# Kernel tuning notes

Hardware: AMD Instinct MI355X
Metric: run time of the kernel (lower is better)

## Reference

```python
import jax, jax.numpy as jnp
import numpy as np

E = 16          # expert_num
T = 8192        # token_num
H = 1024        # hidden_size
I = 4096        # intermediate_size
LN_EPS = 1e-12


def setup_inputs() -> dict:
    key = jax.random.key(0)
    ks = jax.random.split(key, 6)
    hidden_states = jax.random.normal(ks[0], (T, H), dtype=jnp.float32)
    perm = jax.random.permutation(ks[1], T).astype(jnp.int32)
    s1 = 1.0 / np.sqrt(H)
    s2 = 1.0 / np.sqrt(I)
    w1 = jax.random.uniform(ks[2], (E, I, H), jnp.float32, -s1, s1)
    b1 = jax.random.uniform(ks[3], (E, I), jnp.float32, -s1, s1)
    w2 = jax.random.uniform(ks[4], (E, H, I), jnp.float32, -s2, s2)
    b2 = jax.random.uniform(ks[5], (E, H), jnp.float32, -s2, s2)
    ln_gamma = jnp.ones((H,), jnp.float32)
    ln_beta = jnp.zeros((H,), jnp.float32)
    return {"hidden_states": hidden_states, "perm": perm, "w1": w1, "b1": b1,
            "w2": w2, "b2": b2, "ln_gamma": ln_gamma, "ln_beta": ln_beta}


def _layer_norm(x, gamma, beta, eps):
    mu = jnp.mean(x, axis=-1, keepdims=True)
    var = jnp.var(x, axis=-1, keepdims=True)
    return (x - mu) * jax.lax.rsqrt(var + eps) * gamma + beta


def reference(hidden_states, perm, w1, b1, w2, b2, ln_gamma, ln_beta):
    # dispatch: gather tokens by random permutation, group per expert
    xp = hidden_states[perm].reshape(E, T // E, H)            # [E, T/E, H]
    # grouped expert FFN (batched GEMM replaces the per-expert Python loop)
    h = jnp.einsum('eth,eih->eti', xp, w1) + b1[:, None, :]   # [E, T/E, I]
    h = jax.nn.gelu(h, approximate=False)
    o = jnp.einsum('eti,ehi->eth', h, w2) + b2[:, None, :]    # [E, T/E, H]
    # scatter-restore via inverse permutation
    restore = jnp.argsort(perm)
    o = o.reshape(T, H)[restore]
    # dropout is identity (p=0, eval); residual + LayerNorm
    return _layer_norm(o + hidden_states, ln_gamma, ln_beta, LN_EPS)
```

## Files before the change

### kernel.cpp

```cpp
#include <hip/hip_runtime.h>
#include <hip/hip_bf16.h>
#include <stdint.h>

#define E_NUM 16
#define T_NUM 8192
#define H_DIM 1024
#define I_DIM 4096
#define MPE   512

typedef __attribute__((ext_vector_type(8))) short short8;
typedef __attribute__((ext_vector_type(4))) float f32x4;
using bf16 = __hip_bfloat16;

typedef const __attribute__((address_space(1))) void GLV;
typedef __attribute__((address_space(3))) void LDSV;

__device__ __forceinline__ uint32_t pack2_bf16(float a, float b) {
  union { float f; uint32_t u; } ua, ub;
  ua.f = a; ub.f = b;
  uint32_t x = ua.u + (0x7FFFu + ((ua.u >> 16) & 1u));
  uint32_t y = ub.u + (0x7FFFu + ((ub.u >> 16) & 1u));
  return (x >> 16) | (y & 0xFFFF0000u);
}

__device__ __forceinline__ short8 cvt8(f32x4 a, f32x4 b) {
  union { short8 s; __hip_bfloat162 h[4]; } r;
  r.h[0] = __float22bfloat162_rn({a[0], a[1]});
  r.h[1] = __float22bfloat162_rn({a[2], a[3]});
  r.h[2] = __float22bfloat162_rn({b[0], b[1]});
  r.h[3] = __float22bfloat162_rn({b[2], b[3]});
  return r.s;
}

__device__ __forceinline__ float fast_gelu(float x) {
  const float p = x * fmaf(x * x, -0.0713548162726f, -1.59576912161f);
  return x * __builtin_amdgcn_rcpf(1.0f + __expf(p));
}

__global__ __launch_bounds__(256)
void gather_cast_kernel(const float* __restrict__ hs, const int* __restrict__ perm,
                        uint32_t* __restrict__ xp) {
  const int r = blockIdx.x;
  const int t = threadIdx.x;
  const int src = perm[r];
  float4 v = ((const float4*)(hs + (size_t)src * H_DIM))[t];
  uint2 o;
  o.x = pack2_bf16(v.x, v.y);
  o.y = pack2_bf16(v.z, v.w);
  ((uint2*)(xp + (size_t)r * (H_DIM / 2)))[t] = o;
}

template<int LOG_NBN, int NWG>
__global__ __launch_bounds__(512, 2)
void moe_g1_kernel(const bf16* __restrict__ A, const float* __restrict__ Bw,
                   const float* __restrict__ bias, bf16* __restrict__ Hout) {
  constexpr int N = I_DIM, K = H_DIM;
  constexpr int NK = K / 32;
  __shared__ bf16  As[2][128 * 64];
  __shared__ float Bs[2][128 * 32];

  constexpr int qx = NWG >> 3;
  const int orig = blockIdx.x;
  const int wg = (orig & 7) * qx + (orig >> 3);
  const int bm = wg & 1;
  const int bn = (wg >> 1) & ((1 << LOG_NBN) - 1);
  const int e  = wg >> (1 + LOG_NBN);

  const int tid = threadIdx.x;
  const int l = tid & 63;
  const int wv = tid >> 6;
  const int wr = wv >> 1, wc = wv & 1;
  const int fr = l & 15, fq = l >> 4;
  const int rx = fr & 7;

  const bf16*  Ae = A  + ((size_t)e * MPE + (size_t)bm * 256) * K;
  const float* Be = Bw + ((size_t)e * N + (size_t)bn * 128) * K;

  const int p0 = tid >> 3;
  const int ga = (tid & 7) ^ (p0 & 7);
  const bf16* As0 = Ae + (size_t)(p0      + 128 * (ga >> 2)) * K + (ga & 3) * 8;
  const bf16* As1 = Ae + (size_t)(p0 + 64 + 128 * (ga >> 2)) * K + (ga & 3) * 8;
  const float* Bs0 = Be + (size_t)p0 * K + ga * 4;
  const float* Bs1 = Be + (size_t)(p0 + 64) * K + ga * 4;

#define STAGE1(buf, kt)                                                            \
  {                                                                                \
    __builtin_amdgcn_global_load_lds((GLV*)(As0 + (kt) * 32),                      \
        (LDSV*)((char*)&As[buf][0] + tid * 16), 16, 0, 0);                         \
    __builtin_amdgcn_global_load_lds((GLV*)(As1 + (kt) * 32),                      \
        (LDSV*)((char*)&As[buf][0] + 8192 + tid * 16), 16, 0, 0);                  \
    __builtin_amdgcn_global_load_lds((GLV*)(Bs0 + (kt) * 32),                      \
        (LDSV*)((char*)&Bs[buf][0] + tid * 16), 16, 0, 0);                         \
    __builtin_amdgcn_global_load_lds((GLV*)(Bs1 + (kt) * 32),                      \
        (LDSV*)((char*)&Bs[buf][0] + 8192 + tid * 16), 16, 0, 0);                  \
  }

  const int aoff  = ((wr & 1) * 64 + fr) * 128 + ((((wr >> 1) << 2) | fq) ^ rx) * 16;
  const int b0off = (wc * 64 + fr) * 128 + (((fq << 1)) ^ rx) * 16;
  const int b1off = (wc * 64 + fr) * 128 + (((fq << 1) | 1) ^ rx) * 16;

  f32x4 acc[4][4];
#pragma unroll
  for (int m = 0; m < 4; ++m)
#pragma unroll
    for (int n = 0; n < 4; ++n) acc[m][n] = (f32x4){0.f, 0.f, 0.f, 0.f};

  STAGE1(0, 0);
  __syncthreads();

  for (int t = 0; t < NK; ++t) {
    const int cur = t & 1;
    if (t + 1 < NK) STAGE1(cur ^ 1, t + 1);

    short8 a8[4];
#pragma unroll
    for (int m = 0; m < 4; ++m)
      a8[m] = *(const short8*)((const char*)&As[cur][0] + aoff + m * 2048);
    short8 b8[4];
#pragma unroll
    for (int n = 0; n < 4; ++n) {
      const f32x4 x0 = *(const f32x4*)((const char*)&Bs[cur][0] + b0off + n * 2048);
      const f32x4 x1 = *(const f32x4*)((const char*)&Bs[cur][0] + b1off + n * 2048);
      b8[n] = cvt8(x0, x1);
    }
#pragma unroll
    for (int m = 0; m < 4; ++m)
#pragma unroll
      for (int n = 0; n < 4; ++n)
        acc[m][n] = __builtin_amdgcn_mfma_f32_16x16x32_bf16(a8[m], b8[n], acc[m][n], 0, 0, 0);

    __syncthreads();
  }
#undef STAGE1

  float bv[4];
#pragma unroll
  for (int n = 0; n < 4; ++n)
    bv[n] = bias[(size_t)e * N + bn * 128 + wc * 64 + n * 16 + fr];

  bf16* He = Hout + (size_t)e * MPE * N;
#pragma unroll
  for (int m = 0; m < 4; ++m) {
#pragma unroll
    for (int j = 0; j < 4; ++j) {
      const int row = bm * 256 + wr * 64 + m * 16 + fq * 4 + j;
#pragma unroll
      for (int n = 0; n < 4; ++n) {
        const int col = bn * 128 + wc * 64 + n * 16 + fr;
        He[(size_t)row * N + col] = __float2bfloat16(fast_gelu(acc[m][n][j] + bv[n]));
      }
    }
  }
}

template<int KSPLIT, int N, int KFULL, int KLEN, int LOG_NBN>
__global__ __launch_bounds__(1024, 4)
void moe_g2_kernel(const bf16* __restrict__ A, const float* __restrict__ Bw,
                   float* __restrict__ Pout) {
  constexpr int NK = KLEN / 32;
  __shared__ bf16  As[2][512 * 32];
  __shared__ float Bs[2][128 * 32];

  const int nwg = gridDim.x, qx = nwg >> 3, orig = blockIdx.x;
  const int wg = (orig & 7) * qx + (orig >> 3);
  const int bn   = wg & ((1 << LOG_NBN) - 1);
  const int rest = wg >> LOG_NBN;
  const int ks = (KSPLIT == 2) ? (rest & 1) : 0;
  const int e  = (KSPLIT == 2) ? (rest >> 1) : rest;
  const int K0 = ks * KLEN;

  const int tid = threadIdx.x;
  const int l = tid & 63;
  const int w = tid >> 6;
  const int wr = w >> 1, wc = w & 1;
  const int fr = l & 15, fq = l >> 4;
  const int rx = fr & 7;

  const bf16*  Ae = A  + (size_t)e * MPE * KFULL + K0;
  const float* Be = Bw + ((size_t)e * N + (size_t)bn * 128) * KFULL + K0;

  const int apq = tid >> 3;
  const int ag  = (tid & 7) ^ (apq & 7);
  const bf16* As0 = Ae + (size_t)(apq       + 256 * (ag >> 2)) * KFULL + (ag & 3) * 8;
  const bf16* As1 = Ae + (size_t)(apq + 128 + 256 * (ag >> 2)) * KFULL + (ag & 3) * 8;
  const float* Bsrc = Be + (size_t)(tid >> 3) * KFULL + ((tid & 7) ^ ((tid >> 3) & 7)) * 4;

  const int aso = (((((wr >> 2) << 2)) | fq) ^ rx) * 8;
  const int bp0 = (((fq << 1))     ^ rx) * 4;
  const int bp1 = (((fq << 1) | 1) ^ rx) * 4;

#define STAGE2(buf, kt)                                                             \
  {                                                                                 \
    __builtin_amdgcn_global_load_lds((GLV*)(As0 + (kt) * 32),                       \
                                     (LDSV*)&As[buf][tid * 8], 16, 0, 0);           \
    __builtin_amdgcn_global_load_lds((GLV*)(As1 + (kt) * 32),                       \
                                     (LDSV*)&As[buf][(1024 + tid) * 8], 16, 0, 0);  \
    __builtin_amdgcn_global_load_lds((GLV*)(Bsrc + (kt) * 32),                      \
                                     (LDSV*)&Bs[buf][tid * 4], 16, 0, 0);           \
  }

  f32x4 acc[4][4];
#pragma unroll
  for (int m = 0; m < 4; ++m)
#pragma unroll
    for (int n = 0; n < 4; ++n) acc[m][n] = (f32x4){0.f, 0.f, 0.f, 0.f};

  STAGE2(0, 0);
  __syncthreads();

  for (int t = 0; t < NK; ++t) {
    const int cur = t & 1;
    if (t + 1 < NK) STAGE2(cur ^ 1, t + 1);

    short8 a8[4];
#pragma unroll
    for (int m = 0; m < 4; ++m)
      a8[m] = *(const short8*)&As[cur][((wr & 3) * 64 + m * 16 + fr) * 64 + aso];
#pragma unroll
    for (int n = 0; n < 4; ++n) {
      const int col = wc * 64 + n * 16 + fr;
      const f32x4 x0 = *(const f32x4*)&Bs[cur][col * 32 + bp0];
      const f32x4 x1 = *(const f32x4*)&Bs[cur][col * 32 + bp1];
      const short8 b8 = cvt8(x0, x1);
#pragma unroll
      for (int m = 0; m < 4; ++m)
        acc[m][n] = __builtin_amdgcn_mfma_f32_16x16x32_bf16(a8[m], b8, acc[m][n], 0, 0, 0);
    }
    __syncthreads();
  }
#undef STAGE2

  float* Pd = Pout + (size_t)ks * T_NUM * H_DIM + (size_t)e * MPE * N;
#pragma unroll
  for (int m = 0; m < 4; ++m) {
#pragma unroll
    for (int j = 0; j < 4; ++j) {
      const int row = wr * 64 + m * 16 + fq * 4 + j;
#pragma unroll
      for (int n = 0; n < 4; ++n) {
        const int col = bn * 128 + wc * 64 + n * 16 + fr;
        Pd[(size_t)row * N + col] = acc[m][n][j];
      }
    }
  }
}

__global__ __launch_bounds__(256)
void ln_resid2_kernel(float* __restrict__ out, const float* __restrict__ hs,
                      const float* __restrict__ p0, const float* __restrict__ p1,
                      const float* __restrict__ b2, const float* __restrict__ gamma,
                      const float* __restrict__ beta, const int* __restrict__ perm,
                      const int two) {
  const int r = blockIdx.x;
  const int t = threadIdx.x;
  const int e = r >> 9;
  const int drow = perm[r];
  float4 a = ((const float4*)(p0 + (size_t)r * H_DIM))[t];
  if (two) {
    float4 b = ((const float4*)(p1 + (size_t)r * H_DIM))[t];
    a.x += b.x; a.y += b.y; a.z += b.z; a.w += b.w;
  }
  float4 bb = ((const float4*)(b2 + (size_t)e * H_DIM))[t];
  float4 h  = ((const float4*)(hs + (size_t)drow * H_DIM))[t];
  float v0 = a.x + bb.x + h.x, v1 = a.y + bb.y + h.y;
  float v2 = a.z + bb.z + h.z, v3 = a.w + bb.w + h.w;
  float s  = v0 + v1 + v2 + v3;
  float sq = v0 * v0 + v1 * v1 + v2 * v2 + v3 * v3;
#pragma unroll
  for (int off = 32; off > 0; off >>= 1) {
    s  += __shfl_down(s, off);
    sq += __shfl_down(sq, off);
  }
  __shared__ float ss[4], ssq[4];
  const int wv = t >> 6;
  if ((t & 63) == 0) { ss[wv] = s; ssq[wv] = sq; }
  __syncthreads();
  s  = ss[0] + ss[1] + ss[2] + ss[3];
  sq = ssq[0] + ssq[1] + ssq[2] + ssq[3];
  const float mu  = s * (1.0f / (float)H_DIM);
  const float var = sq * (1.0f / (float)H_DIM) - mu * mu;
  const float rs  = rsqrtf(var + 1e-12f);
  float4 g = ((const float4*)gamma)[t];
  float4 b = ((const float4*)beta)[t];
  float4 rr;
  rr.x = (v0 - mu) * rs * g.x + b.x;
  rr.y = (v1 - mu) * rs * g.y + b.y;
  rr.z = (v2 - mu) * rs * g.z + b.z;
  rr.w = (v3 - mu) * rs * g.w + b.w;
  ((float4*)(out + (size_t)drow * H_DIM))[t] = rr;
}

extern "C" void kernel_launch(void* const* d_in, const int* in_sizes, int n_in,
                              void* d_out, int out_size, void* d_ws, size_t ws_size,
                              hipStream_t stream) {
  const float* hs    = (const float*)d_in[0];
  const int*   perm  = (const int*)d_in[1];
  const float* w1    = (const float*)d_in[2];
  const float* b1    = (const float*)d_in[3];
  const float* w2    = (const float*)d_in[4];
  const float* b2    = (const float*)d_in[5];
  const float* gamma = (const float*)d_in[6];
  const float* beta  = (const float*)d_in[7];
  float* out = (float*)d_out;

  const size_t xp_b   = (size_t)T_NUM * H_DIM * sizeof(bf16);
  const size_t hbuf_b = (size_t)T_NUM * I_DIM * sizeof(bf16);
  const size_t part_b = (size_t)T_NUM * H_DIM * sizeof(float);

  bf16*  xp   = (bf16*)d_ws;
  bf16*  hbuf = (bf16*)((char*)d_ws + xp_b);
  float* pbuf = (float*)((char*)d_ws + xp_b + hbuf_b);

  gather_cast_kernel<<<T_NUM, 256, 0, stream>>>(hs, perm, (uint32_t*)xp);

  moe_g1_kernel<5, 1024><<<1024, 512, 0, stream>>>(xp, w1, b1, hbuf);

  if (ws_size >= xp_b + hbuf_b + 2 * part_b) {
    moe_g2_kernel<2, H_DIM, I_DIM, I_DIM / 2, 3>
        <<<256, 1024, 0, stream>>>(hbuf, w2, pbuf);
    ln_resid2_kernel<<<T_NUM, 256, 0, stream>>>(out, hs, pbuf, pbuf + (size_t)T_NUM * H_DIM,
                                                b2, gamma, beta, perm, 1);
  } else {
    moe_g2_kernel<1, H_DIM, I_DIM, I_DIM, 3>
        <<<128, 1024, 0, stream>>>(hbuf, w2, pbuf);
    ln_resid2_kernel<<<T_NUM, 256, 0, stream>>>(out, hs, pbuf, nullptr,
                                                b2, gamma, beta, perm, 0);
  }
}
```

Baseline: 331.8 us.

## Overlap w2 bf16 cast with GEMM1 and use bf16 GEMM2 with fused scatter

The GEMM1 launch now has double the blocks, and the odd-indexed blocks convert w2 from fp32 to bf16 in the workspace while the even blocks run the GEMM. A new bf16×bf16 GEMM2 reads the converted weights at half the bytes, with no split-K. It adds bias and scatters rows straight to the output through perm, so the partial-sum buffers go away. A simpler residual+LayerNorm pass then runs in place. The cast traffic competes with GEMM1 for bandwidth, the co-scheduling depends on block dispatch order, and the path needs a 208MB workspace.

```diff
diff --git a/kernel.cpp b/kernel.cpp
--- a/kernel.cpp
+++ b/kernel.cpp
@@ -50,23 +50,41 @@
   ((uint2*)(xp + (size_t)r * (H_DIM / 2)))[t] = o;
 }
 
-template<int LOG_NBN, int NWG>
+template<int LOG_NBN>
 __global__ __launch_bounds__(512, 2)
-void moe_g1_kernel(const bf16* __restrict__ A, const float* __restrict__ Bw,
-                   const float* __restrict__ bias, bf16* __restrict__ Hout) {
+void moe_g1_cast_kernel(const bf16* __restrict__ A, const float* __restrict__ Bw,
+                        const float* __restrict__ bias, bf16* __restrict__ Hout,
+                        const float* __restrict__ csrc, uint32_t* __restrict__ cdst,
+                        long n4) {
   constexpr int N = I_DIM, K = H_DIM;
   constexpr int NK = K / 32;
   __shared__ bf16  As[2][128 * 64];
   __shared__ float Bs[2][128 * 32];
 
-  constexpr int qx = NWG >> 3;
   const int orig = blockIdx.x;
-  const int wg = (orig & 7) * qx + (orig >> 3);
-  const int bm = wg & 1;
-  const int bn = (wg >> 1) & ((1 << LOG_NBN) - 1);
-  const int e  = wg >> (1 + LOG_NBN);
-
+  const int xcd = orig & 7;
+  const int s = orig >> 3;
   const int tid = threadIdx.x;
+
+  if (s & 1) {
+    const long cid = xcd * 128 + (s >> 1);
+    long i = cid * 512 + tid;
+    const long step = 1024 * 512;
+    for (; i < n4; i += step) {
+      float4 v = ((const float4*)csrc)[i];
+      uint2 o;
+      o.x = pack2_bf16(v.x, v.y);
+      o.y = pack2_bf16(v.z, v.w);
+      ((uint2*)cdst)[i] = o;
+    }
+    return;
+  }
+
+  const int gid = xcd * 128 + (s >> 1);
+  const int bm = gid & 1;
+  const int bn = (gid >> 1) & ((1 << LOG_NBN) - 1);
+  const int e  = gid >> (1 + LOG_NBN);
+
   const int l = tid & 63;
   const int wv = tid >> 6;
   const int wr = wv >> 1, wc = wv & 1;
@@ -153,10 +171,107 @@
   }
 }
 
+template<int N, int K, int LOG_NBN, int NWG>
+__global__ __launch_bounds__(256, 2)
+void moe_g2_b16_kernel(const bf16* __restrict__ A, const bf16* __restrict__ Bw,
+                       const float* __restrict__ bias, float* __restrict__ Oout,
+                       const int* __restrict__ perm) {
+  constexpr int NK = K / 64;
+  __shared__ bf16 As[2][128 * 64];
+  __shared__ bf16 Bs[2][128 * 64];
+
+  constexpr int qx = NWG >> 3;
+  const int orig = blockIdx.x;
+  const int wg = (orig & 7) * qx + (orig >> 3);
+  const int bm = wg & 3;
+  const int bn = (wg >> 2) & ((1 << LOG_NBN) - 1);
+  const int e  = wg >> (2 + LOG_NBN);
+
+  const int tid = threadIdx.x;
+  const int l = tid & 63;
+  const int wv = tid >> 6;
+  const int wr = wv >> 1, wc = wv & 1;
+  const int fr = l & 15, fq = l >> 4;
+  const int rx = fr & 7;
+
+  const bf16* Ae = A  + ((size_t)e * MPE + (size_t)bm * 128) * K;
+  const bf16* Be = Bw + ((size_t)e * N + (size_t)bn * 128) * K;
+
+  const int sr = tid >> 3;
+  const int swz = ((tid & 7) ^ (sr & 7)) << 3;
+  const bf16* Asrc = Ae + (size_t)sr * K + swz;
+  const bf16* Bsrc = Be + (size_t)sr * K + swz;
+
+#define STAGE_B16(buf, kt)                                                          \
+  {                                                                                 \
+    _Pragma("unroll")                                                               \
+    for (int i = 0; i < 4; ++i)                                                     \
+      __builtin_amdgcn_global_load_lds((GLV*)(Asrc + (size_t)i * 32 * K + (kt) * 64), \
+                                       (LDSV*)&As[buf][(i * 256 + wv * 64) * 8], 16, 0, 0); \
+    _Pragma("unroll")                                                               \
+    for (int i = 0; i < 4; ++i)                                                     \
+      __builtin_amdgcn_global_load_lds((GLV*)(Bsrc + (size_t)i * 32 * K + (kt) * 64), \
+                                       (LDSV*)&Bs[buf][(i * 256 + wv * 64) * 8], 16, 0, 0); \
+  }
+
+  f32x4 acc[4][4];
+#pragma unroll
+  for (int m = 0; m < 4; ++m)
+#pragma unroll
+    for (int n = 0; n < 4; ++n) acc[m][n] = (f32x4){0.f, 0.f, 0.f, 0.f};
+
+  STAGE_B16(0, 0);
+  __syncthreads();
+
+  for (int t = 0; t < NK; ++t) {
+    const int cur = t & 1, nxt = cur ^ 1;
+    if (t + 1 < NK) STAGE_B16(nxt, t + 1);
+
+#pragma unroll
+    for (int kk = 0; kk < 2; ++kk) {
+      const int ch = ((kk * 4 + fq) ^ rx) << 3;
+      short8 a8[4], b8[4];
+#pragma unroll
+      for (int m = 0; m < 4; ++m)
+        a8[m] = *(const short8*)&As[cur][(wr * 64 + m * 16 + fr) * 64 + ch];
+#pragma unroll
+      for (int n = 0; n < 4; ++n)
+        b8[n] = *(const short8*)&Bs[cur][(wc * 64 + n * 16 + fr) * 64 + ch];
+#pragma unroll
+      for (int m = 0; m < 4; ++m)
+#pragma unroll
+        for (int n = 0; n < 4; ++n)
+          acc[m][n] = __builtin_amdgcn_mfma_f32_16x16x32_bf16(a8[m], b8[n], acc[m][n], 0, 0, 0);
+    }
+    __syncthreads();
+  }
+#undef STAGE_B16
+
+  float bv[4];
+#pragma unroll
+  for (int n = 0; n < 4; ++n)
+    bv[n] = bias[(size_t)e * N + bn * 128 + wc * 64 + n * 16 + fr];
+
+#pragma unroll
+  for (int m = 0; m < 4; ++m) {
+#pragma unroll
+    for (int j = 0; j < 4; ++j) {
+      const int grow = e * MPE + bm * 128 + wr * 64 + m * 16 + fq * 4 + j;
+      const int drow = perm[grow];
+      float* orow = Oout + (size_t)drow * N;
+#pragma unroll
+      for (int n = 0; n < 4; ++n) {
+        const int col = bn * 128 + wc * 64 + n * 16 + fr;
+        orow[col] = acc[m][n][j] + bv[n];
+      }
+    }
+  }
+}
+
 template<int KSPLIT, int N, int KFULL, int KLEN, int LOG_NBN>
 __global__ __launch_bounds__(1024, 4)
-void moe_g2_kernel(const bf16* __restrict__ A, const float* __restrict__ Bw,
-                   float* __restrict__ Pout) {
+void moe_g2_f32_kernel(const bf16* __restrict__ A, const float* __restrict__ Bw,
+                       float* __restrict__ Pout) {
   constexpr int NK = KLEN / 32;
   __shared__ bf16  As[2][512 * 32];
   __shared__ float Bs[2][128 * 32];
@@ -243,6 +358,40 @@
       }
     }
   }
+}
+
+__global__ __launch_bounds__(256)
+void ln_resid_kernel(float* __restrict__ out, const float* __restrict__ hs,
+                     const float* __restrict__ gamma, const float* __restrict__ beta) {
+  const int r = blockIdx.x;
+  const int t = threadIdx.x;
+  float4 o = ((const float4*)(out + (size_t)r * H_DIM))[t];
+  float4 h = ((const float4*)(hs  + (size_t)r * H_DIM))[t];
+  float v0 = o.x + h.x, v1 = o.y + h.y, v2 = o.z + h.z, v3 = o.w + h.w;
+  float s  = v0 + v1 + v2 + v3;
+  float sq = v0 * v0 + v1 * v1 + v2 * v2 + v3 * v3;
+#pragma unroll
+  for (int off = 32; off > 0; off >>= 1) {
+    s  += __shfl_down(s, off);
+    sq += __shfl_down(sq, off);
+  }
+  __shared__ float ss[4], ssq[4];
+  const int wv = t >> 6;
+  if ((t & 63) == 0) { ss[wv] = s; ssq[wv] = sq; }
+  __syncthreads();
+  s  = ss[0] + ss[1] + ss[2] + ss[3];
+  sq = ssq[0] + ssq[1] + ssq[2] + ssq[3];
+  const float mu  = s * (1.0f / (float)H_DIM);
+  const float var = sq * (1.0f / (float)H_DIM) - mu * mu;
+  const float rs  = rsqrtf(var + 1e-12f);
+  float4 g = ((const float4*)gamma)[t];
+  float4 b = ((const float4*)beta)[t];
+  float4 rr;
+  rr.x = (v0 - mu) * rs * g.x + b.x;
+  rr.y = (v1 - mu) * rs * g.y + b.y;
+  rr.z = (v2 - mu) * rs * g.z + b.z;
+  rr.w = (v3 - mu) * rs * g.w + b.w;
+  ((float4*)(out + (size_t)r * H_DIM))[t] = rr;
 }
 
 __global__ __launch_bounds__(256)
@@ -303,27 +452,39 @@
   const float* beta  = (const float*)d_in[7];
   float* out = (float*)d_out;
 
-  const size_t xp_b   = (size_t)T_NUM * H_DIM * sizeof(bf16);
-  const size_t hbuf_b = (size_t)T_NUM * I_DIM * sizeof(bf16);
-  const size_t part_b = (size_t)T_NUM * H_DIM * sizeof(float);
-
-  bf16*  xp   = (bf16*)d_ws;
-  bf16*  hbuf = (bf16*)((char*)d_ws + xp_b);
-  float* pbuf = (float*)((char*)d_ws + xp_b + hbuf_b);
+  const size_t MB = 1024ull * 1024ull;
+  const long n4w2 = (long)E_NUM * H_DIM * I_DIM / 4;
+
+  bf16* xp   = (bf16*)d_ws;
+  bf16* hbuf = (bf16*)((char*)d_ws + 16 * MB);
 
   gather_cast_kernel<<<T_NUM, 256, 0, stream>>>(hs, perm, (uint32_t*)xp);
 
-  moe_g1_kernel<5, 1024><<<1024, 512, 0, stream>>>(xp, w1, b1, hbuf);
-
-  if (ws_size >= xp_b + hbuf_b + 2 * part_b) {
-    moe_g2_kernel<2, H_DIM, I_DIM, I_DIM / 2, 3>
-        <<<256, 1024, 0, stream>>>(hbuf, w2, pbuf);
-    ln_resid2_kernel<<<T_NUM, 256, 0, stream>>>(out, hs, pbuf, pbuf + (size_t)T_NUM * H_DIM,
-                                                b2, gamma, beta, perm, 1);
+  if (ws_size >= 208 * MB) {
+    bf16* w2b = (bf16*)((char*)d_ws + 80 * MB);
+    moe_g1_cast_kernel<5><<<2048, 512, 0, stream>>>(
+        xp, w1, b1, hbuf, w2, (uint32_t*)w2b, n4w2);
+    moe_g2_b16_kernel<H_DIM, I_DIM, 3, 512><<<512, 256, 0, stream>>>(
+        hbuf, w2b, b2, out, perm);
+    ln_resid_kernel<<<T_NUM, 256, 0, stream>>>(out, hs, gamma, beta);
   } else {
-    moe_g2_kernel<1, H_DIM, I_DIM, I_DIM, 3>
-        <<<128, 1024, 0, stream>>>(hbuf, w2, pbuf);
-    ln_resid2_kernel<<<T_NUM, 256, 0, stream>>>(out, hs, pbuf, nullptr,
-                                                b2, gamma, beta, perm, 0);
-  }
-}
+    const size_t xp_b   = (size_t)T_NUM * H_DIM * sizeof(bf16);
+    const size_t hbuf_b = (size_t)T_NUM * I_DIM * sizeof(bf16);
+    const size_t part_b = (size_t)T_NUM * H_DIM * sizeof(float);
+    float* pbuf = (float*)((char*)d_ws + xp_b + hbuf_b);
+    moe_g1_cast_kernel<5><<<2048, 512, 0, stream>>>(
+        xp, w1, b1, hbuf, nullptr, nullptr, 0);
+    if (ws_size >= xp_b + hbuf_b + 2 * part_b) {
+      moe_g2_f32_kernel<2, H_DIM, I_DIM, I_DIM / 2, 3>
+          <<<256, 1024, 0, stream>>>(hbuf, w2, pbuf);
+      ln_resid2_kernel<<<T_NUM, 256, 0, stream>>>(out, hs, pbuf,
+                                                  pbuf + (size_t)T_NUM * H_DIM,
+                                                  b2, gamma, beta, perm, 1);
+    } else {
+      moe_g2_f32_kernel<1, H_DIM, I_DIM, I_DIM, 3>
+          <<<128, 1024, 0, stream>>>(hbuf, w2, pbuf);
+      ln_resid2_kernel<<<T_NUM, 256, 0, stream>>>(out, hs, pbuf, nullptr,
+                                                  b2, gamma, beta, perm, 0);
+    }
+  }
+}
```

Measured after the change: 439.1 us. 32.3% more time.
